# Kernel optimization log

Hardware: AMD Instinct MI355X
Metric: run time of the kernel (lower is better)

The kernel has to match this reference:

```python
import jax, jax.numpy as jnp
import numpy as np

B, CIN, COUT, KH, KW = 8, 64, 128, 3, 3
H = W = 64
STRIDE, PAD = 1, 1
G = 1  # deformable groups


def setup_inputs() -> dict:
    key = jax.random.key(0)
    k1, k2, k3 = jax.random.split(key, 3)
    rgb = jax.random.normal(k1, (B, CIN, H, W), dtype=jnp.float32)
    # torchvision layout: [B, 2*G*KH*KW, Ho, Wo], (dy, dx) pairs per kernel tap
    offsets = jax.random.normal(k2, (B, 2 * G * KH * KW, H, W), dtype=jnp.float32)
    # xavier_uniform for weight [COUT, CIN, KH, KW]
    fan_in, fan_out = CIN * KH * KW, COUT * KH * KW
    a = float(np.sqrt(6.0 / (fan_in + fan_out)))
    weight = jax.random.uniform(k3, (COUT, CIN, KH, KW), dtype=jnp.float32, minval=-a, maxval=a)
    bias = jnp.zeros((COUT,), dtype=jnp.float32)
    return {"rgb": rgb, "offsets": offsets, "weight": weight, "bias": bias}


def _deform_conv2d(rgb, offsets, weight, bias):
    b, cin, h, w = rgb.shape
    cout, _, kh, kw = weight.shape
    K = kh * kw
    ho = (h + 2 * PAD - kh) // STRIDE + 1
    wo = (w + 2 * PAD - kw) // STRIDE + 1
    cg = cin // G  # channels per deformable group

    off = offsets.reshape(b, G, K, 2, ho, wo)
    dy, dx = off[:, :, :, 0], off[:, :, :, 1]  # [b, G, K, ho, wo]

    ky, kx = jnp.meshgrid(jnp.arange(kh), jnp.arange(kw), indexing="ij")
    ky = ky.reshape(K).astype(jnp.float32)
    kx = kx.reshape(K).astype(jnp.float32)
    base_y = (jnp.arange(ho) * STRIDE - PAD).astype(jnp.float32)
    base_x = (jnp.arange(wo) * STRIDE - PAD).astype(jnp.float32)

    # sampling coordinates: p0 + kernel tap + learned offset -> [b, G, K, ho, wo]
    y = base_y[None, None, None, :, None] + ky[None, None, :, None, None] + dy
    x = base_x[None, None, None, None, :] + kx[None, None, :, None, None] + dx

    y0 = jnp.floor(y)
    x0 = jnp.floor(x)
    fy = y - y0
    fx = x - x0
    y0i = y0.astype(jnp.int32)
    x0i = x0.astype(jnp.int32)

    x_flat = rgb.reshape(b, G, cg, h * w)
    P = K * ho * wo

    def gather_corner(yc, xc, wgt):
        valid = (yc >= 0) & (yc < h) & (xc >= 0) & (xc < w)
        idx = jnp.clip(yc, 0, h - 1) * w + jnp.clip(xc, 0, w - 1)
        wgt = jnp.where(valid, wgt, 0.0).reshape(b, G, 1, P)
        vals = jnp.take_along_axis(x_flat, idx.reshape(b, G, 1, P), axis=3)
        return vals * wgt

    col = (
        gather_corner(y0i, x0i, (1 - fy) * (1 - fx))
        + gather_corner(y0i, x0i + 1, (1 - fy) * fx)
        + gather_corner(y0i + 1, x0i, fy * (1 - fx))
        + gather_corner(y0i + 1, x0i + 1, fy * fx)
    )  # [b, G, cg, K*ho*wo]

    col = col.reshape(b, cin * K, ho * wo)
    out = jnp.einsum("ok,bkp->bop", weight.reshape(cout, cin * K), col)
    return out.reshape(b, cout, ho, wo) + bias[None, :, None, None]


def reference(rgb, offsets, weight, bias):
    return _deform_conv2d(rgb, offsets, weight, bias)
```

## Files before the change

### kernel.cpp

```cpp
#include <hip/hip_runtime.h>

#define COUT_  128
#define KP     1024
#define CAPR   16
#define IMGP   (17 * 64)
#define IMGBUF (2 * IMGP)
#define COLW   20
#define COLBUF (32 * COLW)
#define WS_NEED (size_t)(COUT_ * KP * 2 + 8ull * 64 * 64 * 64 * 4)

#if __has_builtin(__builtin_amdgcn_fdot2_f32_bf16)
#define HAS_DOT2 1
#else
#define HAS_DOT2 0
#endif

typedef __attribute__((ext_vector_type(8))) __bf16 bf16x8;
typedef __attribute__((ext_vector_type(2))) __bf16 bf16x2;
typedef unsigned short u16x8 __attribute__((ext_vector_type(8)));
typedef __attribute__((ext_vector_type(4))) float f32x4;

__device__ __forceinline__ unsigned int f2bf(float f) {
    union { float f; unsigned int u; } c; c.f = f;
    unsigned int u = c.u;
    u += 0x7fffu + ((u >> 16) & 1u);
    return u >> 16;
}
__device__ __forceinline__ float bitsf(unsigned int u) {
    union { unsigned int u; float f; } c; c.u = u; return c.f;
}
__device__ __forceinline__ unsigned int pk2bf(float lo, float hi) {
    return f2bf(lo) | (f2bf(hi) << 16);
}
__device__ __forceinline__ bf16x2 mk_bf2(float lo, float hi) {
    unsigned int u = pk2bf(lo, hi);
    return __builtin_bit_cast(bf16x2, u);
}
__device__ __forceinline__ void gl_lds16(const unsigned int* g, unsigned int* l) {
    __builtin_amdgcn_global_load_lds(
        (const __attribute__((address_space(1))) unsigned int*)g,
        (__attribute__((address_space(3))) unsigned int*)l, 16, 0, 0);
}

__global__ void prep_all(const float* __restrict__ w, unsigned short* __restrict__ wbf,
                         const float* __restrict__ rgb, unsigned int* __restrict__ rgbp,
                         int do_rgb) {
    const int bx = blockIdx.x;
    if (bx < 512) {
        int idx = bx * 256 + threadIdx.x;
        int cout = idx >> 10, r = idx & 1023;
        int pair = r >> 5, j2 = r & 31;
        int k = j2 >> 1, par = j2 & 1;
        unsigned short v = 0;
        if (j2 < 18) v = (unsigned short)f2bf(w[(cout * 64 + pair * 2 + par) * 9 + k]);
        wbf[idx] = v;
    } else if (do_rgb) {
        int idx = (bx - 512) * 256 + threadIdx.x;
        float a = rgb[idx];
        float nb = ((idx & 63) == 63) ? 0.f : rgb[idx + 1];
        rgbp[idx] = f2bf(a) | (f2bf(nb) << 16);
    }
}

template<bool PREP>
__launch_bounds__(256, 4)
__global__ void deform_mfma9(const float* __restrict__ rgb,
                             const unsigned int* __restrict__ rgbp,
                             const float* __restrict__ off,
                             const unsigned short* __restrict__ wbf,
                             const float* __restrict__ bias,
                             float* __restrict__ out) {
    __shared__ unsigned int S[2 * COLBUF + 2 * IMGBUF];
    __shared__ int sYmin, sYmax;
    unsigned int* imgU = S + 2 * COLBUF;

    const int t    = threadIdx.x;
    const int bid  = blockIdx.x;
    const int b    = bid & 7;
    const int ho   = (bid >> 3) & 63;
    const int px0  = (bid >> 9) * 32;
    const int lane = t & 63;
    const int wv   = t >> 6;
    const int px   = t & 31;
    const int tg   = t >> 5;
    const int ln15 = lane & 15;
    const int q    = lane >> 4;

    const float* offb = off + b * (2 * 9 * 4096);

    {
        uint4* S4 = (uint4*)S;
        const int n4 = (2 * COLBUF + 2 * IMGBUF) / 4;
        for (int i = t; i < n4; i += 256) S4[i] = make_uint4(0, 0, 0, 0);
    }
    if (t == 0) { sYmin = 64; sYmax = -1; }
    __syncthreads();

    float m_fy[2], m_fx[2]; int m_y0[2], m_x0[2];
    int lmin = 64, lmax = -1;
#pragma unroll
    for (int ti = 0; ti < 2; ti++) {
        const int kt = ti ? 8 : tg;
        const int wo = px0 + px;
        const float dy = offb[((2 * kt)     * 64 + ho) * 64 + wo];
        const float dx = offb[((2 * kt + 1) * 64 + ho) * 64 + wo];
        const float y = (float)(ho - 1 + kt / 3) + dy;
        const float x = (float)(wo - 1 + kt % 3) + dx;
        const float y0f = floorf(y), x0f = floorf(x);
        m_fy[ti] = y - y0f; m_fx[ti] = x - x0f;
        m_y0[ti] = (int)y0f; m_x0[ti] = (int)x0f;
        const int r0 = min(max(m_y0[ti], 0), 63), r1 = min(max(m_y0[ti] + 1, 0), 63);
        lmin = min(lmin, r0); lmax = max(lmax, r1);
    }
    atomicMin(&sYmin, lmin); atomicMax(&sYmax, lmax);
    __syncthreads();
    const int ymin  = sYmin;
    const int nrows = sYmax - ymin + 1;
    const int nr4   = min((nrows + 3) & ~3, CAPR);
    const int ymin2 = max(0, min(ymin, 64 - nr4));

    auto stage_dma = [&](int gg) {
#pragma unroll
        for (int u = 0; u < 2; u++) {
            const int c = wv + u * 4;
            const int plane = c >> 2, r4 = (c & 3) * 4;
            if (r4 < nr4) {
                const unsigned int* gp = rgbp
                    + ((unsigned)(b * 64 + gg * 2 + plane) * 64 + ymin2 + r4) * 64 + lane * 4;
                unsigned int* lp = imgU + (gg & 1) * IMGBUF + plane * IMGP + r4 * 64;
                gl_lds16(gp, lp);
            }
        }
    };
    float4 sv[2];
    auto stage_load = [&](int gg) {
#pragma unroll
        for (int u = 0; u < 2; u++) {
            const int c = wv + u * 4;
            const int plane = c >> 2, r4 = (c & 3) * 4;
            if (r4 < nr4)
                sv[u] = *(const float4*)(rgb
                    + ((unsigned)(b * 64 + gg * 2 + plane) * 64 + ymin2 + r4 + (lane >> 4)) * 64
                    + (lane & 15) * 4);
        }
    };
    auto stage_write = [&](int gg) {
#pragma unroll
        for (int u = 0; u < 2; u++) {
            const int c = wv + u * 4;
            const int plane = c >> 2, r4 = (c & 3) * 4;
            const float4 v = sv[u];
            unsigned int b0 = f2bf(v.x), b1 = f2bf(v.y), b2 = f2bf(v.z), b3 = f2bf(v.w);
            unsigned int nb = __shfl(b0, lane + 1);
            if ((lane & 15) == 15) nb = 0;
            if (r4 < nr4) {
                uint4 pk;
                pk.x = b0 | (b1 << 16); pk.y = b1 | (b2 << 16);
                pk.z = b2 | (b3 << 16); pk.w = b3 | (nb << 16);
                *(uint4*)(imgU + (gg & 1) * IMGBUF + plane * IMGP
                          + (r4 + (lane >> 4)) * 64 + (lane & 15) * 4) = pk;
            }
        }
    };

    int ma[2];
#if HAS_DOT2
    bf16x2 wtp[2], wbp[2];
#else
    float mw[2][4];
#endif
#pragma unroll
    for (int ti = 0; ti < 2; ti++) {
        const int y0 = m_y0[ti], x0 = m_x0[ti];
        const float fy = m_fy[ti], fx = m_fx[ti];
        const int r0 = y0 - ymin2;
        const float wy0 = (y0 >= 0  && y0 < 64) ? (1.f - fy) : 0.f;
        const float wy1 = (y0 >= -1 && y0 < 63) ? fy         : 0.f;
        const bool ylo = (r0 < 0);
        const float wtop = ylo ? wy1 : wy0;
        const float wbot = ylo ? 0.f : wy1;
        const int r0c = ylo ? 0 : min(r0, nr4 - 1);
        const float wx0 = (x0 >= 0  && x0 < 64) ? (1.f - fx) : 0.f;
        const float wx1 = (x0 >= -1 && x0 < 63) ? fx         : 0.f;
        const bool xlo = (x0 < 0);
        const float wA = xlo ? wx1 : wx0;
        const float wB = xlo ? 0.f : wx1;
        const int xc = min(max(x0, 0), 63);
        ma[ti] = r0c * 64 + xc;
#if HAS_DOT2
        wtp[ti] = mk_bf2(wtop * wA, wtop * wB);
        wbp[ti] = mk_bf2(wbot * wA, wbot * wB);
#else
        mw[ti][0] = wtop * wA; mw[ti][1] = wtop * wB;
        mw[ti][2] = wbot * wA; mw[ti][3] = wbot * wB;
#endif
    }

    f32x4 acc[2][2] = {};
    const unsigned short* wrow0 = wbf + (wv * 32 + ln15) * KP;
    const unsigned short* wrow1 = wrow0 + 16 * KP;
    const unsigned short* col16 = (const unsigned short*)S;

    auto interp1 = [&](const unsigned int* pl, int ti) -> float {
        const unsigned int* p = pl + ma[ti];
        const unsigned int tp = p[0];
        const unsigned int bp = p[64];
#if HAS_DOT2
        float r = __builtin_amdgcn_fdot2_f32_bf16(__builtin_bit_cast(bf16x2, tp), wtp[ti], 0.f, false);
        return  __builtin_amdgcn_fdot2_f32_bf16(__builtin_bit_cast(bf16x2, bp), wbp[ti], r, false);
#else
        return mw[ti][0] * bitsf(tp << 16) + mw[ti][1] * bitsf(tp & 0xffff0000u)
             + mw[ti][2] * bitsf(bp << 16) + mw[ti][3] * bitsf(bp & 0xffff0000u);
#endif
    };
    auto gather = [&](int g) {
        const unsigned int* ib = imgU + (g & 1) * IMGBUF;
        unsigned int* cb = S + (g & 1) * COLBUF + px * COLW;
        cb[tg] = pk2bf(interp1(ib, 0), interp1(ib + IMGP, 0));
        if (tg == (g & 7))
            cb[8] = pk2bf(interp1(ib, 1), interp1(ib + IMGP, 1));
    };
    auto mfma_step = [&](int g, u16x8 a0u, u16x8 a1u) {
        const bf16x8 a0 = __builtin_bit_cast(bf16x8, a0u);
        const bf16x8 a1 = __builtin_bit_cast(bf16x8, a1u);
        const unsigned short* cp = col16 + (g & 1) * (COLBUF * 2) + q * 8;
#pragma unroll
        for (int nj = 0; nj < 2; nj++) {
            const u16x8 bu = *(const u16x8*)(cp + (nj * 16 + ln15) * (COLW * 2));
            const bf16x8 bv = __builtin_bit_cast(bf16x8, bu);
            acc[0][nj] = __builtin_amdgcn_mfma_f32_16x16x32_bf16(a0, bv, acc[0][nj], 0, 0, 0);
            acc[1][nj] = __builtin_amdgcn_mfma_f32_16x16x32_bf16(a1, bv, acc[1][nj], 0, 0, 0);
        }
    };

    if (PREP) stage_dma(0); else { stage_load(0); stage_write(0); }
    __syncthreads();

    u16x8 pA0 = {}, pA1 = {};
    for (int g = 0; g < 32; g++) {
        if (g + 1 < 32) { if (PREP) stage_dma(g + 1); else stage_load(g + 1); }
        u16x8 nA0 = *(const u16x8*)(wrow0 + g * 32 + q * 8);
        u16x8 nA1 = *(const u16x8*)(wrow1 + g * 32 + q * 8);
        if (g > 0) mfma_step(g - 1, pA0, pA1);
        gather(g);
        if (!PREP && g + 1 < 32) stage_write(g + 1);
        __syncthreads();
        pA0 = nA0; pA1 = nA1;
    }
    mfma_step(31, pA0, pA1);

#pragma unroll
    for (int mi = 0; mi < 2; mi++) {
#pragma unroll
        for (int r = 0; r < 4; r++) {
            const int cout = wv * 32 + mi * 16 + q * 4 + r;
            const float bv = bias[cout];
            float* orow = out + ((b * COUT_ + cout) * 64 + ho) * 64 + px0;
#pragma unroll
            for (int nj = 0; nj < 2; nj++)
                orow[nj * 16 + ln15] = acc[mi][nj][r] + bv;
        }
    }
}

extern "C" void kernel_launch(void* const* d_in, const int* in_sizes, int n_in,
                              void* d_out, int out_size, void* d_ws, size_t ws_size,
                              hipStream_t stream) {
    const float* rgb  = (const float*)d_in[0];
    const float* off  = (const float*)d_in[1];
    const float* w    = (const float*)d_in[2];
    const float* bias = (const float*)d_in[3];
    float* out = (float*)d_out;
    unsigned short* wbf = (unsigned short*)d_ws;
    unsigned int* rgbp  = (unsigned int*)((char*)d_ws + COUT_ * KP * 2);

    const int do_rgb = (ws_size >= WS_NEED) ? 1 : 0;
    prep_all<<<do_rgb ? 8704 : 512, 256, 0, stream>>>(w, wbf, rgb, rgbp, do_rgb);
    if (do_rgb)
        deform_mfma9<true><<<1024, 256, 0, stream>>>(rgb, rgbp, off, wbf, bias, out);
    else
        deform_mfma9<false><<<1024, 256, 0, stream>>>(rgb, nullptr, off, wbf, bias, out);
}
```

Before: 116.4 us.

## Restructure deform conv to gather straight into MFMA B-fragments, full-row blocks

Each block now handles a full 64-pixel output row and all 128 output channels, so the grid is halved. Each wave owns 16 pixels and interpolates samples directly into register B-fragments instead of writing a column tile to LDS and reading it back. Weights are pre-permuted into the MFMA A-fragment layout and streamed from global memory. Each stage brings in 8 channel planes, giving 8 iterations with larger double-buffered image tiles. The trade-off is more LDS and registers per block (launch bounds lowered to 2) and one A-fragment global load per MFMA.

```diff
diff --git a/kernel.cpp b/kernel.cpp
--- a/kernel.cpp
+++ b/kernel.cpp
@@ -1,13 +1,10 @@
 #include <hip/hip_runtime.h>
 
 #define COUT_  128
-#define KP     1024
 #define CAPR   16
 #define IMGP   (17 * 64)
-#define IMGBUF (2 * IMGP)
-#define COLW   20
-#define COLBUF (32 * COLW)
-#define WS_NEED (size_t)(COUT_ * KP * 2 + 8ull * 64 * 64 * 64 * 4)
+#define IMGBUF (8 * IMGP)
+#define WS_NEED (size_t)(131072 * 2 + 8ull * 64 * 64 * 64 * 4)
 
 #if __has_builtin(__builtin_amdgcn_fdot2_f32_bf16)
 #define HAS_DOT2 1
@@ -18,6 +15,7 @@
 typedef __attribute__((ext_vector_type(8))) __bf16 bf16x8;
 typedef __attribute__((ext_vector_type(2))) __bf16 bf16x2;
 typedef unsigned short u16x8 __attribute__((ext_vector_type(8)));
+typedef unsigned int u32x4 __attribute__((ext_vector_type(4)));
 typedef __attribute__((ext_vector_type(4))) float f32x4;
 
 __device__ __forceinline__ unsigned int f2bf(float f) {
@@ -47,12 +45,17 @@
                          int do_rgb) {
     const int bx = blockIdx.x;
     if (bx < 512) {
-        int idx = bx * 256 + threadIdx.x;
-        int cout = idx >> 10, r = idx & 1023;
-        int pair = r >> 5, j2 = r & 31;
-        int k = j2 >> 1, par = j2 & 1;
+        int idx  = bx * 256 + threadIdx.x;
+        int j    = idx & 7;
+        int lane = (idx >> 3) & 63;
+        int mt   = (idx >> 9) & 7;
+        int s    = idx >> 12;
+        int ln15 = lane & 15, q = lane >> 4;
+        int j2   = q * 8 + j;
+        int tap  = j2 >> 1, par = j2 & 1;
         unsigned short v = 0;
-        if (j2 < 18) v = (unsigned short)f2bf(w[(cout * 64 + pair * 2 + par) * 9 + k]);
+        if (j2 < 18)
+            v = (unsigned short)f2bf(w[((mt * 16 + ln15) * 64 + s * 2 + par) * 9 + tap]);
         wbf[idx] = v;
     } else if (do_rgb) {
         int idx = (bx - 512) * 256 + threadIdx.x;
@@ -63,54 +66,52 @@
 }
 
 template<bool PREP>
-__launch_bounds__(256, 4)
-__global__ void deform_mfma9(const float* __restrict__ rgb,
-                             const unsigned int* __restrict__ rgbp,
-                             const float* __restrict__ off,
-                             const unsigned short* __restrict__ wbf,
-                             const float* __restrict__ bias,
-                             float* __restrict__ out) {
-    __shared__ unsigned int S[2 * COLBUF + 2 * IMGBUF];
+__launch_bounds__(256, 2)
+__global__ void deform_mfma10(const float* __restrict__ rgb,
+                              const unsigned int* __restrict__ rgbp,
+                              const float* __restrict__ off,
+                              const unsigned short* __restrict__ wbf,
+                              const float* __restrict__ bias,
+                              float* __restrict__ out) {
+    __shared__ unsigned int S[2 * IMGBUF];
     __shared__ int sYmin, sYmax;
-    unsigned int* imgU = S + 2 * COLBUF;
 
     const int t    = threadIdx.x;
     const int bid  = blockIdx.x;
     const int b    = bid & 7;
-    const int ho   = (bid >> 3) & 63;
-    const int px0  = (bid >> 9) * 32;
+    const int ho   = bid >> 3;
     const int lane = t & 63;
     const int wv   = t >> 6;
-    const int px   = t & 31;
-    const int tg   = t >> 5;
     const int ln15 = lane & 15;
     const int q    = lane >> 4;
+    const int px   = wv * 16 + ln15;
 
     const float* offb = off + b * (2 * 9 * 4096);
 
     {
         uint4* S4 = (uint4*)S;
-        const int n4 = (2 * COLBUF + 2 * IMGBUF) / 4;
-        for (int i = t; i < n4; i += 256) S4[i] = make_uint4(0, 0, 0, 0);
+        for (int i = t; i < (2 * IMGBUF) / 4; i += 256) S4[i] = make_uint4(0, 0, 0, 0);
     }
     if (t == 0) { sYmin = 64; sYmax = -1; }
     __syncthreads();
 
-    float m_fy[2], m_fx[2]; int m_y0[2], m_x0[2];
+    float m_fy[4], m_fx[4]; int m_y0[4], m_x0[4], m_live[4];
     int lmin = 64, lmax = -1;
 #pragma unroll
-    for (int ti = 0; ti < 2; ti++) {
-        const int kt = ti ? 8 : tg;
-        const int wo = px0 + px;
-        const float dy = offb[((2 * kt)     * 64 + ho) * 64 + wo];
-        const float dx = offb[((2 * kt + 1) * 64 + ho) * 64 + wo];
-        const float y = (float)(ho - 1 + kt / 3) + dy;
-        const float x = (float)(wo - 1 + kt % 3) + dx;
-        const float y0f = floorf(y), x0f = floorf(x);
-        m_fy[ti] = y - y0f; m_fx[ti] = x - x0f;
-        m_y0[ti] = (int)y0f; m_x0[ti] = (int)x0f;
-        const int r0 = min(max(m_y0[ti], 0), 63), r1 = min(max(m_y0[ti] + 1, 0), 63);
-        lmin = min(lmin, r0); lmax = max(lmax, r1);
+    for (int ti = 0; ti < 4; ti++) {
+        const int kt = q * 4 + ti;
+        m_live[ti] = (kt <= 8);
+        if (kt <= 8) {
+            const float dy = offb[((2 * kt)     * 64 + ho) * 64 + px];
+            const float dx = offb[((2 * kt + 1) * 64 + ho) * 64 + px];
+            const float y = (float)(ho - 1 + kt / 3) + dy;
+            const float x = (float)(px - 1 + kt % 3) + dx;
+            const float y0f = floorf(y), x0f = floorf(x);
+            m_fy[ti] = y - y0f; m_fx[ti] = x - x0f;
+            m_y0[ti] = (int)y0f; m_x0[ti] = (int)x0f;
+            const int r0 = min(max(m_y0[ti], 0), 63), r1 = min(max(m_y0[ti] + 1, 0), 63);
+            lmin = min(lmin, r0); lmax = max(lmax, r1);
+        } else { m_fy[ti] = 0.f; m_fx[ti] = 0.f; m_y0[ti] = 0; m_x0[ti] = 0; }
     }
     atomicMin(&sYmin, lmin); atomicMax(&sYmax, lmax);
     __syncthreads();
@@ -119,36 +120,34 @@
     const int nr4   = min((nrows + 3) & ~3, CAPR);
     const int ymin2 = max(0, min(ymin, 64 - nr4));
 
-    auto stage_dma = [&](int gg) {
+    auto stage_dma = [&](int g) {
 #pragma unroll
         for (int u = 0; u < 2; u++) {
-            const int c = wv + u * 4;
-            const int plane = c >> 2, r4 = (c & 3) * 4;
-            if (r4 < nr4) {
-                const unsigned int* gp = rgbp
-                    + ((unsigned)(b * 64 + gg * 2 + plane) * 64 + ymin2 + r4) * 64 + lane * 4;
-                unsigned int* lp = imgU + (gg & 1) * IMGBUF + plane * IMGP + r4 * 64;
-                gl_lds16(gp, lp);
-            }
-        }
-    };
-    float4 sv[2];
-    auto stage_load = [&](int gg) {
-#pragma unroll
-        for (int u = 0; u < 2; u++) {
-            const int c = wv + u * 4;
-            const int plane = c >> 2, r4 = (c & 3) * 4;
+            const int pl = 2 * wv + u;
+            const unsigned int* gp = rgbp + ((unsigned)(b * 64 + g * 8 + pl) * 64 + ymin2) * 64 + lane * 4;
+            unsigned int* lp = S + (g & 1) * IMGBUF + pl * IMGP;
+#pragma unroll
+            for (int c = 0; c < 4; c++) {
+                const int r4 = c * 4;
+                if (r4 < nr4) gl_lds16(gp + r4 * 64, lp + r4 * 64);
+            }
+        }
+    };
+    float4 sv[8];
+    auto stage_load = [&](int g) {
+#pragma unroll
+        for (int u = 0; u < 8; u++) {
+            const int pl = 2 * wv + (u >> 2), r4 = (u & 3) * 4;
             if (r4 < nr4)
                 sv[u] = *(const float4*)(rgb
-                    + ((unsigned)(b * 64 + gg * 2 + plane) * 64 + ymin2 + r4 + (lane >> 4)) * 64
+                    + ((unsigned)(b * 64 + g * 8 + pl) * 64 + ymin2 + r4 + (lane >> 4)) * 64
                     + (lane & 15) * 4);
         }
     };
-    auto stage_write = [&](int gg) {
-#pragma unroll
-        for (int u = 0; u < 2; u++) {
-            const int c = wv + u * 4;
-            const int plane = c >> 2, r4 = (c & 3) * 4;
+    auto stage_write = [&](int g) {
+#pragma unroll
+        for (int u = 0; u < 8; u++) {
+            const int pl = 2 * wv + (u >> 2), r4 = (u & 3) * 4;
             const float4 v = sv[u];
             unsigned int b0 = f2bf(v.x), b1 = f2bf(v.y), b2 = f2bf(v.z), b3 = f2bf(v.w);
             unsigned int nb = __shfl(b0, lane + 1);
@@ -157,20 +156,20 @@
                 uint4 pk;
                 pk.x = b0 | (b1 << 16); pk.y = b1 | (b2 << 16);
                 pk.z = b2 | (b3 << 16); pk.w = b3 | (nb << 16);
-                *(uint4*)(imgU + (gg & 1) * IMGBUF + plane * IMGP
+                *(uint4*)(S + (g & 1) * IMGBUF + pl * IMGP
                           + (r4 + (lane >> 4)) * 64 + (lane & 15) * 4) = pk;
             }
         }
     };
 
-    int ma[2];
+    int ma[4];
 #if HAS_DOT2
-    bf16x2 wtp[2], wbp[2];
-#else
-    float mw[2][4];
-#endif
-#pragma unroll
-    for (int ti = 0; ti < 2; ti++) {
+    bf16x2 wtp[4], wbp[4];
+#else
+    float mw[4][4];
+#endif
+#pragma unroll
+    for (int ti = 0; ti < 4; ti++) {
         const int y0 = m_y0[ti], x0 = m_x0[ti];
         const float fy = m_fy[ti], fx = m_fx[ti];
         const int r0 = y0 - ymin2;
@@ -196,13 +195,10 @@
 #endif
     }
 
-    f32x4 acc[2][2] = {};
-    const unsigned short* wrow0 = wbf + (wv * 32 + ln15) * KP;
-    const unsigned short* wrow1 = wrow0 + 16 * KP;
-    const unsigned short* col16 = (const unsigned short*)S;
-
-    auto interp1 = [&](const unsigned int* pl, int ti) -> float {
-        const unsigned int* p = pl + ma[ti];
+    f32x4 acc[8] = {};
+
+    auto interp1 = [&](const unsigned int* pl_, int ti) -> float {
+        const unsigned int* p = pl_ + ma[ti];
         const unsigned int tp = p[0];
         const unsigned int bp = p[64];
 #if HAS_DOT2
@@ -213,52 +209,47 @@
              + mw[ti][2] * bitsf(bp << 16) + mw[ti][3] * bitsf(bp & 0xffff0000u);
 #endif
     };
-    auto gather = [&](int g) {
-        const unsigned int* ib = imgU + (g & 1) * IMGBUF;
-        unsigned int* cb = S + (g & 1) * COLBUF + px * COLW;
-        cb[tg] = pk2bf(interp1(ib, 0), interp1(ib + IMGP, 0));
-        if (tg == (g & 7))
-            cb[8] = pk2bf(interp1(ib, 1), interp1(ib + IMGP, 1));
-    };
-    auto mfma_step = [&](int g, u16x8 a0u, u16x8 a1u) {
-        const bf16x8 a0 = __builtin_bit_cast(bf16x8, a0u);
-        const bf16x8 a1 = __builtin_bit_cast(bf16x8, a1u);
-        const unsigned short* cp = col16 + (g & 1) * (COLBUF * 2) + q * 8;
-#pragma unroll
-        for (int nj = 0; nj < 2; nj++) {
-            const u16x8 bu = *(const u16x8*)(cp + (nj * 16 + ln15) * (COLW * 2));
-            const bf16x8 bv = __builtin_bit_cast(bf16x8, bu);
-            acc[0][nj] = __builtin_amdgcn_mfma_f32_16x16x32_bf16(a0, bv, acc[0][nj], 0, 0, 0);
-            acc[1][nj] = __builtin_amdgcn_mfma_f32_16x16x32_bf16(a1, bv, acc[1][nj], 0, 0, 0);
+
+    auto do_group = [&](int g) {
+#pragma unroll
+        for (int ps = 0; ps < 4; ps++) {
+            const int s = g * 4 + ps;
+            const unsigned int* ib = S + (g & 1) * IMGBUF + (2 * ps) * IMGP;
+            unsigned int bw[4];
+#pragma unroll
+            for (int ti = 0; ti < 4; ti++) {
+                bw[ti] = 0u;
+                if (m_live[ti])
+                    bw[ti] = pk2bf(interp1(ib, ti), interp1(ib + IMGP, ti));
+            }
+            u32x4 bv4 = { bw[0], bw[1], bw[2], bw[3] };
+            const bf16x8 bfrag = __builtin_bit_cast(bf16x8, bv4);
+            const unsigned short* abase = wbf + ((unsigned)(s * 8) * 64 + lane) * 8;
+#pragma unroll
+            for (int mt = 0; mt < 8; mt++) {
+                const u16x8 au = *(const u16x8*)(abase + mt * 512);
+                acc[mt] = __builtin_amdgcn_mfma_f32_16x16x32_bf16(
+                    __builtin_bit_cast(bf16x8, au), bfrag, acc[mt], 0, 0, 0);
+            }
         }
     };
 
     if (PREP) stage_dma(0); else { stage_load(0); stage_write(0); }
     __syncthreads();
 
-    u16x8 pA0 = {}, pA1 = {};
-    for (int g = 0; g < 32; g++) {
-        if (g + 1 < 32) { if (PREP) stage_dma(g + 1); else stage_load(g + 1); }
-        u16x8 nA0 = *(const u16x8*)(wrow0 + g * 32 + q * 8);
-        u16x8 nA1 = *(const u16x8*)(wrow1 + g * 32 + q * 8);
-        if (g > 0) mfma_step(g - 1, pA0, pA1);
-        gather(g);
-        if (!PREP && g + 1 < 32) stage_write(g + 1);
+    for (int g = 0; g < 8; g++) {
+        if (g + 1 < 8) { if (PREP) stage_dma(g + 1); else stage_load(g + 1); }
+        do_group(g);
+        if (!PREP && g + 1 < 8) stage_write(g + 1);
         __syncthreads();
-        pA0 = nA0; pA1 = nA1;
-    }
-    mfma_step(31, pA0, pA1);
-
-#pragma unroll
-    for (int mi = 0; mi < 2; mi++) {
+    }
+
+#pragma unroll
+    for (int mt = 0; mt < 8; mt++) {
 #pragma unroll
         for (int r = 0; r < 4; r++) {
-            const int cout = wv * 32 + mi * 16 + q * 4 + r;
-            const float bv = bias[cout];
-            float* orow = out + ((b * COUT_ + cout) * 64 + ho) * 64 + px0;
-#pragma unroll
-            for (int nj = 0; nj < 2; nj++)
-                orow[nj * 16 + ln15] = acc[mi][nj][r] + bv;
+            const int cout = mt * 16 + q * 4 + r;
+            out[((b * COUT_ + cout) * 64 + ho) * 64 + px] = acc[mt][r] + bias[cout];
         }
     }
 }
@@ -272,12 +263,12 @@
     const float* bias = (const float*)d_in[3];
     float* out = (float*)d_out;
     unsigned short* wbf = (unsigned short*)d_ws;
-    unsigned int* rgbp  = (unsigned int*)((char*)d_ws + COUT_ * KP * 2);
+    unsigned int* rgbp  = (unsigned int*)((char*)d_ws + 131072 * 2);
 
     const int do_rgb = (ws_size >= WS_NEED) ? 1 : 0;
     prep_all<<<do_rgb ? 8704 : 512, 256, 0, stream>>>(w, wbf, rgb, rgbp, do_rgb);
     if (do_rgb)
-        deform_mfma9<true><<<1024, 256, 0, stream>>>(rgb, rgbp, off, wbf, bias, out);
+        deform_mfma10<true><<<512, 256, 0, stream>>>(rgb, rgbp, off, wbf, bias, out);
     else
-        deform_mfma9<false><<<1024, 256, 0, stream>>>(rgb, nullptr, off, wbf, bias, out);
-}
+        deform_mfma10<false><<<512, 256, 0, stream>>>(rgb, nullptr, off, wbf, bias, out);
+}
```

Result: slower. 120.9 us (+3.9%).
